# Kernel tuning notes

Hardware: AMD Instinct MI355X
Metric: run time of the kernel (lower is better)

Reference implementation:

```python
import jax, jax.numpy as jnp
import numpy as np

N, E, B, D, R, L = 60000, 600000, 512, 128, 30, 3
CUT_LOW, CUT_HIGH = 0.0, 10.0
N_ATOM_TYPES = 100


def _sp(x, beta, threshold):
    # torch.nn.Softplus(beta, threshold): x if beta*x > threshold else log1p(exp(beta*x))/beta
    bx = beta * x
    return jnp.where(bx > threshold, x, jnp.log1p(jnp.exp(jnp.minimum(bx, threshold))) / beta)


def setup_inputs() -> dict:
    key = jax.random.key(0)
    ks = jax.random.split(key, 16)

    def lin(k, fi, fo):
        k1, k2 = jax.random.split(k)
        W = jax.random.normal(k1, (fi, fo), jnp.float32) * (fi ** -0.5)
        b = jax.random.normal(k2, (fo,), jnp.float32) * 0.01
        return W, b

    def lin_stack(k, fi, fo, n):
        Ws, bs = zip(*[lin(kk, fi, fo) for kk in jax.random.split(k, n)])
        return jnp.stack(Ws), jnp.stack(bs)

    inp = {}
    inp['atom_type'] = jax.random.randint(ks[0], (N,), 0, N_ATOM_TYPES)
    inp['src'] = jax.random.randint(ks[1], (E,), 0, N)
    inp['dst'] = jax.random.randint(ks[2], (E,), 0, N)
    inp['graph_ids'] = jnp.sort(jax.random.randint(ks[3], (N,), 0, B))
    inp['dist'] = jax.random.uniform(ks[4], (E,), jnp.float32) * CUT_HIGH
    inp['node_emb'] = jax.random.normal(ks[5], (N_ATOM_TYPES, D), jnp.float32) * 0.1
    inp['W_n1'], inp['b_n1'] = lin_stack(ks[6], D, D, L)
    inp['W_c1'], inp['b_c1'] = lin_stack(ks[7], R, D, L)
    inp['W_c2'], inp['b_c2'] = lin_stack(ks[8], D, D, L)
    inp['W_c3'], inp['b_c3'] = lin_stack(ks[9], D, D, L)
    inp['W_n2'], inp['b_n2'] = lin_stack(ks[10], D, D, L)
    inp['W_n3'], inp['b_n3'] = lin_stack(ks[11], D, D, L)
    inp['W_r1'], inp['b_r1'] = lin(ks[12], D * (L + 1), 64)
    inp['W_r2'], inp['b_r2'] = lin(ks[13], 64, 1)
    return inp


def reference(atom_type, src, dst, graph_ids, dist, node_emb,
              W_n1, b_n1, W_c1, b_c1, W_c2, b_c2, W_c3, b_c3,
              W_n2, b_n2, W_n3, b_n3, W_r1, b_r1, W_r2, b_r2):
    # RBF expansion of edge distances: exp(-(d - mu_k)^2 / gap)  -> [E, R]
    centers = jnp.linspace(CUT_LOW, CUT_HIGH, R).astype(dist.dtype)
    gap = centers[1] - centers[0]
    rbf = jnp.exp(-((dist[:, None] - centers) ** 2) / gap)

    h = node_emb[atom_type]  # node embedding lookup [N, D]
    hs = [h]
    for i in range(L):  # MultiLevelInteraction layers (fixed small count)
        h_new = hs[-1] @ W_n1[i] + b_n1[i]                       # node_layer1 [N, D]
        # VEConv edge MLP on rbf (linear1 -> softplus(0.5,14) -> linear2 -> linear3)
        e = _sp(rbf @ W_c1[i] + b_c1[i], 0.5, 14.0) @ W_c2[i] + b_c2[i]
        e = e @ W_c3[i] + b_c3[i]                                 # [E, D]
        # sum_e(h_new[src]*e) + sum_e(e) fused into one scatter-sum over dst
        msg = (h_new[src] + 1.0) * e                              # [E, D]
        node = jax.ops.segment_sum(msg, dst, num_segments=N)      # [N, D]
        new_node = _sp(node @ W_n2[i] + b_n2[i], 0.5, 14.0) @ W_n3[i] + b_n3[i]
        hs.append(hs[-1] + new_node)                              # residual h_i
    hcat = jnp.concatenate(hs, axis=1)                            # [N, D*(L+1)]
    out = _sp(hcat @ W_r1 + b_r1, 1.0, 20.0) @ W_r2 + b_r2        # [N, 1]
    # dgl.sum_nodes per molecule, then flatten -> [B]
    return jax.ops.segment_sum(out[:, 0], graph_ids, num_segments=B)
```

## Files before the change

kernel.cpp:

```cpp
#include <hip/hip_runtime.h>
#include <math.h>

#define N_NODES 60000
#define N_EDGES 600000
#define B_GRAPHS 512
#define DIM 128
#define RBF_R 30
#define NLAYERS 3
#define NBINS 1024
#define CHUNK 512
#define NCHUNK ((N_NODES + CHUNK - 1) / CHUNK)

typedef __attribute__((ext_vector_type(8))) short bf16x8;
typedef __attribute__((ext_vector_type(4))) float f32x4;

__device__ __forceinline__ float sp05(float x) {
    float bx = 0.5f * x;
    return bx > 14.0f ? x : 2.0f * log1pf(expf(bx));
}
__device__ __forceinline__ float sp1(float x) {
    return x > 20.0f ? x : log1pf(expf(x));
}
__device__ __forceinline__ unsigned short f2bf(float f) {
    unsigned int u = __float_as_uint(f);
    unsigned int r = u + 0x7FFFu + ((u >> 16) & 1u);
    return (unsigned short)(r >> 16);
}
__device__ __forceinline__ float bf2f(unsigned int s) {
    return __uint_as_float(s << 16);
}

__global__ void k_conv(const float* __restrict__ Wn1, const float* __restrict__ Wn2,
                       const float* __restrict__ Wn3, const float* __restrict__ Wr1,
                       unsigned short* __restrict__ WtF, unsigned short* __restrict__ Wr1tF) {
    int i = blockIdx.x * 256 + threadIdx.x;
    if (i < 9 * 16384) {
        int mat = i >> 14, r = i & 16383;
        int frag = r >> 9, within = r & 511;
        int ks = frag >> 3, ntile = frag & 7;
        int lane = within >> 3, j = within & 7;
        int q = lane >> 4, l16 = lane & 15;
        int n = ntile * 16 + l16;
        int k = ks * 32 + q * 8 + j;
        const float* src = (mat < 3) ? (Wn1 + (size_t)mat * 16384)
                         : (mat < 6) ? (Wn2 + (size_t)(mat - 3) * 16384)
                                     : (Wn3 + (size_t)(mat - 6) * 16384);
        WtF[i] = f2bf(src[k * 128 + n]);
    } else {
        int ii = i - 9 * 16384;
        if (ii < 32768) {
            int frag = ii >> 9, within = ii & 511;
            int lvl = frag >> 4, ks = (frag >> 2) & 3, ntile = frag & 3;
            int lane = within >> 3, j = within & 7;
            int q = lane >> 4, l16 = lane & 15;
            int n = ntile * 16 + l16;
            int k = lvl * 128 + ks * 32 + q * 8 + j;
            Wr1tF[ii] = f2bf(Wr1[k * 64 + n]);
        }
    }
}

__global__ void k_embed(const int* __restrict__ atom_type,
                        const float* __restrict__ node_emb,
                        float* __restrict__ h0, unsigned short* __restrict__ hb0) {
    int i = blockIdx.x * blockDim.x + threadIdx.x;
    if (i >= N_NODES * DIM) return;
    int n = i >> 7, d = i & 127;
    float v = node_emb[atom_type[n] * DIM + d];
    h0[i] = v;
    hb0[i] = f2bf(v);
}


__global__ void k_hist(const int* __restrict__ dst, int* __restrict__ counts) {
    int e = blockIdx.x * blockDim.x + threadIdx.x;
    if (e >= N_EDGES) return;
    atomicAdd(&counts[dst[e]], 1);
}

__global__ void k_bsum(const int* __restrict__ counts, int* __restrict__ bsums) {
    __shared__ int red[256];
    int c = blockIdx.x, tid = threadIdx.x;
    int base = c * CHUNK;
    int v = 0;
    for (int i = tid; i < CHUNK; i += 256)
        if (base + i < N_NODES) v += counts[base + i];
    red[tid] = v;
    __syncthreads();
    for (int s = 128; s > 0; s >>= 1) {
        if (tid < s) red[tid] += red[tid + s];
        __syncthreads();
    }
    if (tid == 0) bsums[c] = red[0];
}

__global__ void k_scan_b(int* __restrict__ bsums) {
    __shared__ int sb[NCHUNK];
    int tid = threadIdx.x;
    if (tid < NCHUNK) sb[tid] = bsums[tid];
    __syncthreads();
    if (tid == 0) {
        int run = 0;
        for (int i = 0; i < NCHUNK; ++i) { int v = sb[i]; sb[i] = run; run += v; }
    }
    __syncthreads();
    if (tid < NCHUNK) bsums[tid] = sb[tid];
}

__global__ void k_scan_final(const int* __restrict__ counts, const int* __restrict__ bsums,
                             int* __restrict__ offsets) {
    __shared__ int sc[CHUNK];
    int c = blockIdx.x, tid = threadIdx.x;
    int base = c * CHUNK;
    for (int i = tid; i < CHUNK; i += 256)
        sc[i] = (base + i < N_NODES) ? counts[base + i] : 0;
    __syncthreads();
    if (tid == 0) {
        int run = bsums[c];
        for (int i = 0; i < CHUNK; ++i) { int v = sc[i]; sc[i] = run; run += v; }
    }
    __syncthreads();
    for (int i = tid; i < CHUNK; i += 256)
        if (base + i < N_NODES) offsets[base + i] = sc[i];
    if (c == 0 && tid == 0) offsets[N_NODES] = N_EDGES;
}

__global__ void k_fill(const int* __restrict__ src, const int* __restrict__ dst,
                       const float* __restrict__ dist,
                       const int* __restrict__ offsets, int* __restrict__ cnt2,
                       uint2* __restrict__ meta) {
    int e = blockIdx.x * blockDim.x + threadIdx.x;
    if (e >= N_EDGES) return;
    int d = dst[e];
    int pos = offsets[d] + atomicAdd(&cnt2[d], 1);
    float x = dist[e];
    float p = x * ((float)NBINS / 10.0f);
    int bin = (int)p;
    if (bin > NBINS - 1) bin = NBINS - 1;
    float w = p - (float)bin;
    int wq = (int)(w * 65535.0f + 0.5f);
    if (wq > 65535) wq = 65535;
    meta[pos] = make_uint2((unsigned)src[e], ((unsigned)bin << 16) | (unsigned)wq);
}


__global__ void k_table_all(const float* __restrict__ Wc1, const float* __restrict__ bc1,
                            const float* __restrict__ Wc2, const float* __restrict__ bc2,
                            const float* __restrict__ Wc3, const float* __restrict__ bc3,
                            unsigned short* __restrict__ tableb) {
    __shared__ float t[DIM];
    __shared__ float u[DIM];
    int lyr = blockIdx.x / (NBINS + 1);
    int b = blockIdx.x % (NBINS + 1);
    int d = threadIdx.x;
    const float* wc1 = Wc1 + (size_t)lyr * RBF_R * DIM;
    const float* wc2 = Wc2 + (size_t)lyr * DIM * DIM;
    const float* wc3 = Wc3 + (size_t)lyr * DIM * DIM;
    float dist = (float)b * (10.0f / (float)NBINS);
    const float gap = 10.0f / 29.0f;
    float acc = bc1[lyr * DIM + d];
#pragma unroll
    for (int k = 0; k < RBF_R; ++k) {
        float c = (float)k * (10.0f / 29.0f);
        float df = dist - c;
        acc += expf(-df * df / gap) * wc1[k * DIM + d];
    }
    t[d] = sp05(acc);
    __syncthreads();
    acc = bc2[lyr * DIM + d];
#pragma unroll 8
    for (int k = 0; k < DIM; ++k) acc += t[k] * wc2[k * DIM + d];
    u[d] = acc;
    __syncthreads();
    acc = bc3[lyr * DIM + d];
#pragma unroll 8
    for (int k = 0; k < DIM; ++k) acc += u[k] * wc3[k * DIM + d];
    tableb[((size_t)lyr * (NBINS + 1) + b) * DIM + d] = f2bf(acc);
}

__global__ void k_pack_all(const unsigned short* __restrict__ tableb,
                           unsigned int* __restrict__ packed) {
    int i = blockIdx.x * 256 + threadIdx.x;
    int lyr = i / (NBINS * DIM);
    int r = i % (NBINS * DIM);
    const unsigned short* tb = tableb + (size_t)lyr * (NBINS + 1) * DIM;
    float a = bf2f(tb[r]);
    float b = bf2f(tb[r + DIM]);
    packed[i] = (unsigned int)f2bf(a) | ((unsigned int)f2bf(b - a) << 16);
}


__global__ __launch_bounds__(256) void k_gemm_g(const unsigned short* __restrict__ Ab,
                                                const unsigned short* __restrict__ WtF,
                                                const float* __restrict__ bias,
                                                unsigned short* __restrict__ Cb) {
    int tid = threadIdx.x;
    int wave = tid >> 6, lane = tid & 63;
    int q = lane >> 4, l16 = lane & 15;
    int mhalf = wave & 1, nhalf = wave >> 1;
    int rb = blockIdx.x * 64 + mhalf * 32;
    int c0 = nhalf * 64;
    bf16x8 bfrag[4][4];
#pragma unroll
    for (int ks = 0; ks < 4; ++ks)
#pragma unroll
        for (int nt = 0; nt < 4; ++nt)
            bfrag[ks][nt] = *(const bf16x8*)&WtF[(size_t)(ks * 8 + nhalf * 4 + nt) * 512 + lane * 8];
    f32x4 acc[2][4] = {};
#pragma unroll
    for (int ks = 0; ks < 4; ++ks)
#pragma unroll
        for (int mt = 0; mt < 2; ++mt) {
            int m = rb + mt * 16 + l16;
            if (m > N_NODES - 1) m = N_NODES - 1;
            bf16x8 a = *(const bf16x8*)&Ab[(size_t)m * 128 + ks * 32 + q * 8];
#pragma unroll
            for (int nt = 0; nt < 4; ++nt)
                acc[mt][nt] = __builtin_amdgcn_mfma_f32_16x16x32_bf16(a, bfrag[ks][nt], acc[mt][nt], 0, 0, 0);
        }
#pragma unroll
    for (int mt = 0; mt < 2; ++mt)
#pragma unroll
        for (int nt = 0; nt < 4; ++nt) {
            int col = c0 + nt * 16 + l16;
            float b = bias[col] + 1.0f;
#pragma unroll
            for (int r = 0; r < 4; ++r) {
                int row = rb + mt * 16 + q * 4 + r;
                if (row < N_NODES) Cb[(size_t)row * 128 + col] = f2bf(acc[mt][nt][r] + b);
            }
        }
}

__global__ __launch_bounds__(256) void k_gather(
    const int* __restrict__ offsets, const uint2* __restrict__ meta,
    const unsigned int* __restrict__ packed, const unsigned short* __restrict__ gb,
    unsigned short* __restrict__ nodeb) {
    int wave = threadIdx.x >> 6, lane = threadIdx.x & 63;
    int n = blockIdx.x * 4 + wave;
    int beg = offsets[n], end = offsets[n + 1];
    int off = lane * 2;
    const float ws = 1.0f / 65535.0f;
    float acc0 = 0.f, acc1 = 0.f, acc2 = 0.f, acc3 = 0.f;
    int j = beg;
    for (; j + 4 <= end; j += 4) {
        uint2 m0 = meta[j], m1 = meta[j + 1], m2 = meta[j + 2], m3 = meta[j + 3];
        uint2 p0 = *(const uint2*)&packed[(size_t)(m0.y >> 16) * DIM + off];
        uint2 p1 = *(const uint2*)&packed[(size_t)(m1.y >> 16) * DIM + off];
        uint2 p2 = *(const uint2*)&packed[(size_t)(m2.y >> 16) * DIM + off];
        uint2 p3 = *(const uint2*)&packed[(size_t)(m3.y >> 16) * DIM + off];
        unsigned int g0 = *(const unsigned int*)&gb[(size_t)m0.x * DIM + off];
        unsigned int g1 = *(const unsigned int*)&gb[(size_t)m1.x * DIM + off];
        unsigned int g2 = *(const unsigned int*)&gb[(size_t)m2.x * DIM + off];
        unsigned int g3 = *(const unsigned int*)&gb[(size_t)m3.x * DIM + off];
        float w0 = (float)(m0.y & 0xffff) * ws;
        float w1 = (float)(m1.y & 0xffff) * ws;
        float w2 = (float)(m2.y & 0xffff) * ws;
        float w3 = (float)(m3.y & 0xffff) * ws;
        acc0 += bf2f(g0 & 0xffff) * (bf2f(p0.x & 0xffff) + w0 * bf2f(p0.x >> 16));
        acc1 += bf2f(g0 >> 16)    * (bf2f(p0.y & 0xffff) + w0 * bf2f(p0.y >> 16));
        acc2 += bf2f(g1 & 0xffff) * (bf2f(p1.x & 0xffff) + w1 * bf2f(p1.x >> 16));
        acc3 += bf2f(g1 >> 16)    * (bf2f(p1.y & 0xffff) + w1 * bf2f(p1.y >> 16));
        acc0 += bf2f(g2 & 0xffff) * (bf2f(p2.x & 0xffff) + w2 * bf2f(p2.x >> 16));
        acc1 += bf2f(g2 >> 16)    * (bf2f(p2.y & 0xffff) + w2 * bf2f(p2.y >> 16));
        acc2 += bf2f(g3 & 0xffff) * (bf2f(p3.x & 0xffff) + w3 * bf2f(p3.x >> 16));
        acc3 += bf2f(g3 >> 16)    * (bf2f(p3.y & 0xffff) + w3 * bf2f(p3.y >> 16));
    }
    for (; j < end; ++j) {
        uint2 m0 = meta[j];
        uint2 p0 = *(const uint2*)&packed[(size_t)(m0.y >> 16) * DIM + off];
        unsigned int g0 = *(const unsigned int*)&gb[(size_t)m0.x * DIM + off];
        float w0 = (float)(m0.y & 0xffff) * ws;
        acc0 += bf2f(g0 & 0xffff) * (bf2f(p0.x & 0xffff) + w0 * bf2f(p0.x >> 16));
        acc1 += bf2f(g0 >> 16)    * (bf2f(p0.y & 0xffff) + w0 * bf2f(p0.y >> 16));
    }
    acc0 += acc2; acc1 += acc3;
    unsigned int o = (unsigned int)f2bf(acc0) | ((unsigned int)f2bf(acc1) << 16);
    *(unsigned int*)&nodeb[(size_t)n * DIM + off] = o;
}

__global__ __launch_bounds__(256) void k_node_update(
    const unsigned short* __restrict__ nodeb,
    const unsigned short* __restrict__ W2tF, const float* __restrict__ b2,
    const unsigned short* __restrict__ W3tF, const float* __restrict__ b3,
    const float* __restrict__ h_in, float* __restrict__ h_out,
    unsigned short* __restrict__ hb_out) {
    __shared__ unsigned short ts[64][136];
    int tid = threadIdx.x;
    int wave = tid >> 6, lane = tid & 63;
    int q = lane >> 4, l16 = lane & 15;
    int mhalf = wave & 1, nhalf = wave >> 1;
    int rb = blockIdx.x * 64 + mhalf * 32;
    int c0 = nhalf * 64;

    bf16x8 bfrag[4][4];
#pragma unroll
    for (int ks = 0; ks < 4; ++ks)
#pragma unroll
        for (int nt = 0; nt < 4; ++nt)
            bfrag[ks][nt] = *(const bf16x8*)&W2tF[(size_t)(ks * 8 + nhalf * 4 + nt) * 512 + lane * 8];
    f32x4 acc[2][4] = {};
#pragma unroll
    for (int ks = 0; ks < 4; ++ks)
#pragma unroll
        for (int mt = 0; mt < 2; ++mt) {
            int m = rb + mt * 16 + l16;
            if (m > N_NODES - 1) m = N_NODES - 1;
            bf16x8 a = *(const bf16x8*)&nodeb[(size_t)m * 128 + ks * 32 + q * 8];
#pragma unroll
            for (int nt = 0; nt < 4; ++nt)
                acc[mt][nt] = __builtin_amdgcn_mfma_f32_16x16x32_bf16(a, bfrag[ks][nt], acc[mt][nt], 0, 0, 0);
        }
#pragma unroll
    for (int mt = 0; mt < 2; ++mt)
#pragma unroll
        for (int nt = 0; nt < 4; ++nt) {
            int col = c0 + nt * 16 + l16;
            float b = b2[col];
#pragma unroll
            for (int r = 0; r < 4; ++r) {
                int lrow = mhalf * 32 + mt * 16 + q * 4 + r;
                ts[lrow][col] = f2bf(sp05(acc[mt][nt][r] + b));
            }
        }
    __syncthreads();
#pragma unroll
    for (int ks = 0; ks < 4; ++ks)
#pragma unroll
        for (int nt = 0; nt < 4; ++nt)
            bfrag[ks][nt] = *(const bf16x8*)&W3tF[(size_t)(ks * 8 + nhalf * 4 + nt) * 512 + lane * 8];
#pragma unroll
    for (int mt = 0; mt < 2; ++mt)
#pragma unroll
        for (int nt = 0; nt < 4; ++nt) acc[mt][nt] = (f32x4){0.f, 0.f, 0.f, 0.f};
#pragma unroll
    for (int ks = 0; ks < 4; ++ks)
#pragma unroll
        for (int mt = 0; mt < 2; ++mt) {
            int lrow = mhalf * 32 + mt * 16 + l16;
            bf16x8 a = *(const bf16x8*)&ts[lrow][ks * 32 + q * 8];
#pragma unroll
            for (int nt = 0; nt < 4; ++nt)
                acc[mt][nt] = __builtin_amdgcn_mfma_f32_16x16x32_bf16(a, bfrag[ks][nt], acc[mt][nt], 0, 0, 0);
        }
#pragma unroll
    for (int mt = 0; mt < 2; ++mt)
#pragma unroll
        for (int nt = 0; nt < 4; ++nt) {
            int col = c0 + nt * 16 + l16;
            float b = b3[col];
#pragma unroll
            for (int r = 0; r < 4; ++r) {
                int row = rb + mt * 16 + q * 4 + r;
                if (row < N_NODES) {
                    size_t idx = (size_t)row * 128 + col;
                    float v = h_in[idx] + acc[mt][nt][r] + b;
                    h_out[idx] = v;
                    hb_out[idx] = f2bf(v);
                }
            }
        }
}

__global__ __launch_bounds__(256) void k_readout(
    const unsigned short* __restrict__ hb0, const unsigned short* __restrict__ hb1,
    const unsigned short* __restrict__ hb2, const unsigned short* __restrict__ hb3,
    const unsigned short* __restrict__ Wr1tF, const float* __restrict__ br1,
    const float* __restrict__ Wr2, const float* __restrict__ br2,
    const int* __restrict__ graph_ids, float* __restrict__ out) {
    int tid = threadIdx.x;
    int wave = tid >> 6, lane = tid & 63;
    int q = lane >> 4, l16 = lane & 15;
    int rb0 = blockIdx.x * 128 + wave * 16;
    const unsigned short* hbs[4] = {hb0, hb1, hb2, hb3};
    f32x4 acc[2][4] = {};
    for (int lvl = 0; lvl < 4; ++lvl) {
        bf16x8 bfrag[4][4];
#pragma unroll
        for (int ks = 0; ks < 4; ++ks)
#pragma unroll
            for (int nt = 0; nt < 4; ++nt)
                bfrag[ks][nt] = *(const bf16x8*)&Wr1tF[(size_t)((lvl * 4 + ks) * 4 + nt) * 512 + lane * 8];
        const unsigned short* Ab = hbs[lvl];
#pragma unroll
        for (int ks = 0; ks < 4; ++ks)
#pragma unroll
            for (int mt = 0; mt < 2; ++mt) {
                int m = rb0 + mt * 64 + l16;
                if (m > N_NODES - 1) m = N_NODES - 1;
                bf16x8 a = *(const bf16x8*)&Ab[(size_t)m * 128 + ks * 32 + q * 8];
#pragma unroll
                for (int nt = 0; nt < 4; ++nt)
                    acc[mt][nt] = __builtin_amdgcn_mfma_f32_16x16x32_bf16(a, bfrag[ks][nt], acc[mt][nt], 0, 0, 0);
            }
    }
    float brr = br2[0];
#pragma unroll
    for (int mt = 0; mt < 2; ++mt) {
        float partial[4] = {0.f, 0.f, 0.f, 0.f};
#pragma unroll
        for (int nt = 0; nt < 4; ++nt) {
            int col = nt * 16 + l16;
            float b = br1[col];
            float w = Wr2[col];
#pragma unroll
            for (int r = 0; r < 4; ++r) partial[r] += sp1(acc[mt][nt][r] + b) * w;
        }
#pragma unroll
        for (int r = 0; r < 4; ++r) {
            float v = partial[r];
            v += __shfl_xor(v, 1); v += __shfl_xor(v, 2);
            v += __shfl_xor(v, 4); v += __shfl_xor(v, 8);
            if (l16 == 0) {
                int row = rb0 + mt * 64 + q * 4 + r;
                if (row < N_NODES) atomicAdd(&out[graph_ids[row]], v + brr);
            }
        }
    }
}

extern "C" void kernel_launch(void* const* d_in, const int* in_sizes, int n_in,
                              void* d_out, int out_size, void* d_ws, size_t ws_size,
                              hipStream_t stream) {
    const int* atom_type   = (const int*)d_in[0];
    const int* src         = (const int*)d_in[1];
    const int* dst         = (const int*)d_in[2];
    const int* graph_ids   = (const int*)d_in[3];
    const float* dist      = (const float*)d_in[4];
    const float* node_emb  = (const float*)d_in[5];
    const float* W_n1 = (const float*)d_in[6];  const float* b_n1 = (const float*)d_in[7];
    const float* W_c1 = (const float*)d_in[8];  const float* b_c1 = (const float*)d_in[9];
    const float* W_c2 = (const float*)d_in[10]; const float* b_c2 = (const float*)d_in[11];
    const float* W_c3 = (const float*)d_in[12]; const float* b_c3 = (const float*)d_in[13];
    const float* W_n2 = (const float*)d_in[14]; const float* b_n2 = (const float*)d_in[15];
    const float* W_n3 = (const float*)d_in[16]; const float* b_n3 = (const float*)d_in[17];
    const float* W_r1 = (const float*)d_in[18]; const float* b_r1 = (const float*)d_in[19];
    const float* W_r2 = (const float*)d_in[20]; const float* b_r2 = (const float*)d_in[21];
    float* out = (float*)d_out;

    size_t ND = (size_t)N_NODES * DIM;
    float* h_even = (float*)d_ws;
    float* h_odd  = h_even + ND;
    uint2* meta   = (uint2*)(h_odd + ND);
    int* offsets  = (int*)(meta + N_EDGES);
    int* counts   = offsets + 60008;
    int* cnt2     = counts + N_NODES;
    int* bsums    = cnt2 + N_NODES;
    unsigned int* packed = (unsigned int*)(bsums + 128);
    unsigned short* hb0    = (unsigned short*)(packed + (size_t)3 * NBINS * DIM);
    unsigned short* hb1    = hb0 + ND;
    unsigned short* hb2    = hb1 + ND;
    unsigned short* hb3    = hb2 + ND;
    unsigned short* gb     = hb3 + ND;
    unsigned short* nodeb  = gb + ND;
    unsigned short* tableb = nodeb + ND;
    unsigned short* WtF    = tableb + (size_t)3 * (NBINS + 1) * DIM;
    unsigned short* Wr1tF  = WtF + 9 * 16384;

    unsigned short* hbp[4] = {hb0, hb1, hb2, hb3};
    float* hcur = h_even;
    float* hnext = h_odd;

    hipMemsetAsync(out, 0, B_GRAPHS * sizeof(float), stream);
    hipMemsetAsync(counts, 0, (2 * N_NODES + 128) * sizeof(int), stream);

    k_conv<<<(9 * 16384 + 32768 + 255) / 256, 256, 0, stream>>>(
        W_n1, W_n2, W_n3, W_r1, WtF, Wr1tF);
    k_embed<<<(N_NODES * DIM) / 256, 256, 0, stream>>>(atom_type, node_emb, h_even, hb0);
    k_table_all<<<3 * (NBINS + 1), DIM, 0, stream>>>(
        W_c1, b_c1, W_c2, b_c2, W_c3, b_c3, tableb);
    k_pack_all<<<(3 * NBINS * DIM) / 256, 256, 0, stream>>>(tableb, packed);

    k_hist<<<(N_EDGES + 255) / 256, 256, 0, stream>>>(dst, counts);
    k_bsum<<<NCHUNK, 256, 0, stream>>>(counts, bsums);
    k_scan_b<<<1, 128, 0, stream>>>(bsums);
    k_scan_final<<<NCHUNK, 256, 0, stream>>>(counts, bsums, offsets);
    k_fill<<<(N_EDGES + 255) / 256, 256, 0, stream>>>(src, dst, dist, offsets, cnt2, meta);

    int gblocks = (N_NODES + 63) / 64;
    int rblocks = (N_NODES + 127) / 128;
    for (int i = 0; i < NLAYERS; ++i) {
        k_gemm_g<<<gblocks, 256, 0, stream>>>(
            hbp[i], WtF + (size_t)i * 16384, b_n1 + (size_t)i * DIM, gb);
        k_gather<<<N_NODES / 4, 256, 0, stream>>>(
            offsets, meta, packed + (size_t)i * NBINS * DIM, gb, nodeb);
        k_node_update<<<gblocks, 256, 0, stream>>>(
            nodeb, WtF + (size_t)(3 + i) * 16384, b_n2 + (size_t)i * DIM,
            WtF + (size_t)(6 + i) * 16384, b_n3 + (size_t)i * DIM,
            hcur, hnext, hbp[i + 1]);
        float* tmp = hcur; hcur = hnext; hnext = tmp;
    }
    k_readout<<<rblocks, 256, 0, stream>>>(
        hb0, hb1, hb2, hb3, Wr1tF, b_r1, W_r2, b_r2, graph_ids, out);
}
```

Measured before the change: 586.6 us.

## Fuse next-layer node GEMM into node update and drop fp32 residual buffers

The node_layer1 GEMM for the next layer now runs inside the node-update kernel, using the freshly computed bf16 hidden state staged in shared memory. This removes a separate kernel launch and a re-read of the hidden state. The fp32 residual stream is removed, and residuals are accumulated from bf16 copies, cutting fp32 read/write traffic at the cost of extra rounding error across layers. The node-update kernel also uses more shared memory, which may reduce occupancy.

```diff
diff --git a/kernel.cpp b/kernel.cpp
--- a/kernel.cpp
+++ b/kernel.cpp
@@ -62,13 +62,11 @@
 
 __global__ void k_embed(const int* __restrict__ atom_type,
                         const float* __restrict__ node_emb,
-                        float* __restrict__ h0, unsigned short* __restrict__ hb0) {
+                        unsigned short* __restrict__ hb0) {
     int i = blockIdx.x * blockDim.x + threadIdx.x;
     if (i >= N_NODES * DIM) return;
     int n = i >> 7, d = i & 127;
-    float v = node_emb[atom_type[n] * DIM + d];
-    h0[i] = v;
-    hb0[i] = f2bf(v);
+    hb0[i] = f2bf(node_emb[atom_type[n] * DIM + d]);
 }
 
 
@@ -283,9 +281,11 @@
     const unsigned short* __restrict__ nodeb,
     const unsigned short* __restrict__ W2tF, const float* __restrict__ b2,
     const unsigned short* __restrict__ W3tF, const float* __restrict__ b3,
-    const float* __restrict__ h_in, float* __restrict__ h_out,
-    unsigned short* __restrict__ hb_out) {
+    const unsigned short* __restrict__ hb_in, unsigned short* __restrict__ hb_out,
+    const unsigned short* __restrict__ WgF, const float* __restrict__ bg,
+    unsigned short* __restrict__ gb, int do_g) {
     __shared__ unsigned short ts[64][136];
+    __shared__ unsigned short hs[64][136];
     int tid = threadIdx.x;
     int wave = tid >> 6, lane = tid & 63;
     int q = lane >> 4, l16 = lane & 15;
@@ -352,12 +352,50 @@
 #pragma unroll
             for (int r = 0; r < 4; ++r) {
                 int row = rb + mt * 16 + q * 4 + r;
+                int lrow = mhalf * 32 + mt * 16 + q * 4 + r;
+                size_t idx = (size_t)row * 128 + col;
+                float v;
                 if (row < N_NODES) {
-                    size_t idx = (size_t)row * 128 + col;
-                    float v = h_in[idx] + acc[mt][nt][r] + b;
-                    h_out[idx] = v;
-                    hb_out[idx] = f2bf(v);
+                    v = bf2f(hb_in[idx]) + acc[mt][nt][r] + b;
+                    unsigned short bf = f2bf(v);
+                    hb_out[idx] = bf;
+                    hs[lrow][col] = bf;
+                } else {
+                    hs[lrow][col] = 0;
                 }
+            }
+        }
+    if (!do_g) return;
+    __syncthreads();
+#pragma unroll
+    for (int ks = 0; ks < 4; ++ks)
+#pragma unroll
+        for (int nt = 0; nt < 4; ++nt)
+            bfrag[ks][nt] = *(const bf16x8*)&WgF[(size_t)(ks * 8 + nhalf * 4 + nt) * 512 + lane * 8];
+#pragma unroll
+    for (int mt = 0; mt < 2; ++mt)
+#pragma unroll
+        for (int nt = 0; nt < 4; ++nt) acc[mt][nt] = (f32x4){0.f, 0.f, 0.f, 0.f};
+#pragma unroll
+    for (int ks = 0; ks < 4; ++ks)
+#pragma unroll
+        for (int mt = 0; mt < 2; ++mt) {
+            int lrow = mhalf * 32 + mt * 16 + l16;
+            bf16x8 a = *(const bf16x8*)&hs[lrow][ks * 32 + q * 8];
+#pragma unroll
+            for (int nt = 0; nt < 4; ++nt)
+                acc[mt][nt] = __builtin_amdgcn_mfma_f32_16x16x32_bf16(a, bfrag[ks][nt], acc[mt][nt], 0, 0, 0);
+        }
+#pragma unroll
+    for (int mt = 0; mt < 2; ++mt)
+#pragma unroll
+        for (int nt = 0; nt < 4; ++nt) {
+            int col = c0 + nt * 16 + l16;
+            float b = bg[col] + 1.0f;
+#pragma unroll
+            for (int r = 0; r < 4; ++r) {
+                int row = rb + mt * 16 + q * 4 + r;
+                if (row < N_NODES) gb[(size_t)row * 128 + col] = f2bf(acc[mt][nt][r] + b);
             }
         }
 }
@@ -439,9 +477,7 @@
     float* out = (float*)d_out;
 
     size_t ND = (size_t)N_NODES * DIM;
-    float* h_even = (float*)d_ws;
-    float* h_odd  = h_even + ND;
-    uint2* meta   = (uint2*)(h_odd + ND);
+    uint2* meta   = (uint2*)d_ws;
     int* offsets  = (int*)(meta + N_EDGES);
     int* counts   = offsets + 60008;
     int* cnt2     = counts + N_NODES;
@@ -458,15 +494,13 @@
     unsigned short* Wr1tF  = WtF + 9 * 16384;
 
     unsigned short* hbp[4] = {hb0, hb1, hb2, hb3};
-    float* hcur = h_even;
-    float* hnext = h_odd;
 
     hipMemsetAsync(out, 0, B_GRAPHS * sizeof(float), stream);
     hipMemsetAsync(counts, 0, (2 * N_NODES + 128) * sizeof(int), stream);
 
     k_conv<<<(9 * 16384 + 32768 + 255) / 256, 256, 0, stream>>>(
         W_n1, W_n2, W_n3, W_r1, WtF, Wr1tF);
-    k_embed<<<(N_NODES * DIM) / 256, 256, 0, stream>>>(atom_type, node_emb, h_even, hb0);
+    k_embed<<<(N_NODES * DIM) / 256, 256, 0, stream>>>(atom_type, node_emb, hb0);
     k_table_all<<<3 * (NBINS + 1), DIM, 0, stream>>>(
         W_c1, b_c1, W_c2, b_c2, W_c3, b_c3, tableb);
     k_pack_all<<<(3 * NBINS * DIM) / 256, 256, 0, stream>>>(tableb, packed);
@@ -479,16 +513,17 @@
 
     int gblocks = (N_NODES + 63) / 64;
     int rblocks = (N_NODES + 127) / 128;
+    k_gemm_g<<<gblocks, 256, 0, stream>>>(hb0, WtF, b_n1, gb);
     for (int i = 0; i < NLAYERS; ++i) {
-        k_gemm_g<<<gblocks, 256, 0, stream>>>(
-            hbp[i], WtF + (size_t)i * 16384, b_n1 + (size_t)i * DIM, gb);
         k_gather<<<N_NODES / 4, 256, 0, stream>>>(
             offsets, meta, packed + (size_t)i * NBINS * DIM, gb, nodeb);
+        int do_g = (i < NLAYERS - 1) ? 1 : 0;
         k_node_update<<<gblocks, 256, 0, stream>>>(
             nodeb, WtF + (size_t)(3 + i) * 16384, b_n2 + (size_t)i * DIM,
             WtF + (size_t)(6 + i) * 16384, b_n3 + (size_t)i * DIM,
-            hcur, hnext, hbp[i + 1]);
-        float* tmp = hcur; hcur = hnext; hnext = tmp;
+            hbp[i], hbp[i + 1],
+            WtF + (size_t)(i + 1) * 16384, b_n1 + (size_t)(i + 1 < 3 ? i + 1 : 0) * DIM,
+            gb, do_g);
     }
     k_readout<<<rblocks, 256, 0, stream>>>(
         hb0, hb1, hb2, hb3, Wr1tF, b_r1, W_r2, b_r2, graph_ids, out);
```

Result: faster. 569.1 us (-3.0%).
